# Kernel optimization log

Measured on AMD Instinct MI355X. Metric: run time of the kernel, lower is better.

Reference implementation:

```python
import jax, jax.numpy as jnp
import numpy as np

N = 100000   # nodes
E = 3200000  # edges per graph
D = 16       # embedding_size, num_heads = 1
ATTN_SLOPE = 0.2   # DGL GATv2Conv negative_slope default
ACT_SLOPE = 0.01   # torch.nn.functional.leaky_relu default (activation arg)


def gatv2_layer(h, src, dst, W_src, b_src, W_dst, b_dst, attn):
    """DGL GATv2Conv with num_heads=1, activation=leaky_relu.
    h: [N, D]; src/dst: [E] int; W_*: [D, D]; b_*: [D]; attn: [D].
    """
    feat_src = h @ W_src + b_src          # [N, D]
    feat_dst = h @ W_dst + b_dst          # [N, D]
    el = feat_src[src]                    # [E, D] gather to edges
    e = jax.nn.leaky_relu(el + feat_dst[dst], ATTN_SLOPE)  # [E, D]
    score = e @ attn                      # [E] attention logits
    # segment softmax over incoming edges of each destination node
    smax = jax.ops.segment_max(score, dst, num_segments=N)
    smax = jnp.where(jnp.isfinite(smax), smax, 0.0)  # empty segments -> 0
    ex = jnp.exp(score - smax[dst])       # [E]
    denom = jax.ops.segment_sum(ex, dst, num_segments=N)  # [N]
    alpha = ex / denom[dst]               # [E]
    rst = jax.ops.segment_sum(alpha[:, None] * el, dst, num_segments=N)  # [N, D]
    return jax.nn.leaky_relu(rst, ACT_SLOPE)


def setup_inputs() -> dict:
    key = jax.random.key(0)
    ks = jax.random.split(key, 16)
    s = 1.0 / np.sqrt(D)
    return {
        "embedding": jax.random.normal(ks[0], (N, D), jnp.float32),
        "src1": jax.random.randint(ks[1], (E,), 0, N, jnp.int32),
        "dst1": jax.random.randint(ks[2], (E,), 0, N, jnp.int32),
        "src2": jax.random.randint(ks[3], (E,), 0, N, jnp.int32),
        "dst2": jax.random.randint(ks[4], (E,), 0, N, jnp.int32),
        "W_src1": jax.random.normal(ks[5], (D, D), jnp.float32) * s,
        "b_src1": jnp.zeros((D,), jnp.float32),
        "W_dst1": jax.random.normal(ks[6], (D, D), jnp.float32) * s,
        "b_dst1": jnp.zeros((D,), jnp.float32),
        "attn1": jax.random.normal(ks[7], (D,), jnp.float32) * s,
        "W_src2": jax.random.normal(ks[8], (D, D), jnp.float32) * s,
        "b_src2": jnp.zeros((D,), jnp.float32),
        "W_dst2": jax.random.normal(ks[9], (D, D), jnp.float32) * s,
        "b_dst2": jnp.zeros((D,), jnp.float32),
        "attn2": jax.random.normal(ks[10], (D,), jnp.float32) * s,
    }


def reference(embedding, src1, dst1, src2, dst2,
              W_src1, b_src1, W_dst1, b_dst1, attn1,
              W_src2, b_src2, W_dst2, b_dst2, attn2):
    user2item = gatv2_layer(embedding, src1, dst1, W_src1, b_src1, W_dst1, b_dst1, attn1)
    item_influence = gatv2_layer(user2item, src2, dst2, W_src2, b_src2, W_dst2, b_dst2, attn2)
    return item_influence  # [N, D]
```

## Files before the change

kernel.cpp:

```cpp
#include <hip/hip_runtime.h>
#include <hip/hip_fp16.h>

#define D 16
#define R 64
#define RBITS 6
#define RMASK 63
#define STRIDE 2560
#define CAP 2560
#define KPT (CAP / 256)
#define EPB 8192
#define SBT 1024
#define NBMAX 2048
#define ATTN_SLOPE 0.2f
#define ACT_SLOPE 0.01f

__device__ __forceinline__ float leaky_a(float v) {
    return v > 0.f ? v : ATTN_SLOPE * v;
}

__device__ __forceinline__ float2 h2f(unsigned u) {
    __half2 h = *(__half2*)&u;
    return __half22float2(h);
}

__device__ __forceinline__ int block_scan_pair(int pair, int tid, int* swsum) {
    int lane = tid & 63, w = tid >> 6;
    int x = pair;
#pragma unroll
    for (int ofs = 1; ofs < 64; ofs <<= 1) {
        int y = __shfl_up(x, ofs, 64);
        if (lane >= ofs) x += y;
    }
    if (lane == 63) swsum[w] = x;
    __syncthreads();
    if (w == 0) {
        int v = (lane < 16) ? swsum[lane] : 0;
        int s = v;
#pragma unroll
        for (int ofs = 1; ofs < 16; ofs <<= 1) {
            int y = __shfl_up(s, ofs, 64);
            if (lane >= ofs) s += y;
        }
        if (lane < 16) swsum[lane] = s - v;
    }
    __syncthreads();
    return x - pair + swsum[w];
}

__global__ void node_transform_kernel(const float* __restrict__ h,
                                      const float* __restrict__ Wsrc,
                                      const float* __restrict__ bsrc,
                                      const float* __restrict__ Wdst,
                                      const float* __restrict__ bdst,
                                      __half* __restrict__ feat_src_h,
                                      float* __restrict__ feat_dst,
                                      int* __restrict__ gcur,
                                      int N, int NB) {
    __shared__ float sWs[D * D], sWd[D * D], sbs[D], sbd[D];
    int t = threadIdx.x;
    if (t < D * D) {
        sWs[t] = Wsrc[t];
        sWd[t] = Wdst[t];
    }
    if (t < D) {
        sbs[t] = bsrc[t];
        sbd[t] = bdst[t];
    }
    int n = blockIdx.x * blockDim.x + t;
    if (n < NB) gcur[n] = n * STRIDE;
    __syncthreads();
    if (n >= N) return;
    float hv[D];
    const float4* h4 = (const float4*)(h + (size_t)n * D);
#pragma unroll
    for (int k = 0; k < 4; k++) {
        float4 v = h4[k];
        hv[4 * k] = v.x; hv[4 * k + 1] = v.y; hv[4 * k + 2] = v.z; hv[4 * k + 3] = v.w;
    }
    float os[D], od[D];
#pragma unroll
    for (int d = 0; d < D; d++) {
        float ss = sbs[d];
        float sd = sbd[d];
#pragma unroll
        for (int k = 0; k < D; k++) {
            ss += hv[k] * sWs[k * D + d];
            sd += hv[k] * sWd[k * D + d];
        }
        os[d] = ss; od[d] = sd;
    }
    unsigned us[8];
#pragma unroll
    for (int k = 0; k < 8; k++) {
        __half2 hh = __floats2half2_rn(os[2 * k], os[2 * k + 1]);
        us[k] = *(unsigned*)&hh;
    }
    uint4* fo = (uint4*)(feat_src_h + (size_t)n * D);
    fo[0] = make_uint4(us[0], us[1], us[2], us[3]);
    fo[1] = make_uint4(us[4], us[5], us[6], us[7]);
    float4* fd4 = (float4*)(feat_dst + (size_t)n * D);
#pragma unroll
    for (int k = 0; k < 4; k++)
        fd4[k] = make_float4(od[4 * k], od[4 * k + 1], od[4 * k + 2], od[4 * k + 3]);
}

__global__ void binscatter_kernel(const int* __restrict__ src, const int* __restrict__ dst,
                                  int* __restrict__ gcur, unsigned* __restrict__ binned,
                                  int E, int NB) {
    __shared__ unsigned sorted[EPB];
    __shared__ unsigned short sposb[EPB];
    __shared__ int shist[NBMAX];
    __shared__ int soffs[NBMAX];
    __shared__ int sgbase[NBMAX];
    __shared__ int swsum[16];
    int tid = threadIdx.x;
    int base = blockIdx.x * EPB;
    int count = E - base;
    if (count > EPB) count = EPB;

    for (int i = tid; i < NB; i += SBT) shist[i] = 0;
    __syncthreads();
    if (base + EPB <= E) {
        const int4* d4 = (const int4*)(dst + base);
#pragma unroll
        for (int k = 0; k < EPB / SBT / 4; k++) {
            int4 v = d4[k * SBT + tid];
            atomicAdd(&shist[v.x >> RBITS], 1);
            atomicAdd(&shist[v.y >> RBITS], 1);
            atomicAdd(&shist[v.z >> RBITS], 1);
            atomicAdd(&shist[v.w >> RBITS], 1);
        }
    } else {
#pragma unroll
        for (int k = 0; k < EPB / SBT; k++) {
            int e = base + k * SBT + tid;
            if (e < E) atomicAdd(&shist[dst[e] >> RBITS], 1);
        }
    }
    __syncthreads();
    int i0 = 2 * tid, i1 = 2 * tid + 1;
    int a0 = (i0 < NB) ? shist[i0] : 0;
    int a1 = (i1 < NB) ? shist[i1] : 0;
    int excl = block_scan_pair(a0 + a1, tid, swsum);
    if (i0 < NB) {
        shist[i0] = excl;
        soffs[i0] = excl;
        if (a0 > 0) sgbase[i0] = atomicAdd(&gcur[i0], a0);
    }
    if (i1 < NB) {
        shist[i1] = excl + a0;
        soffs[i1] = excl + a0;
        if (a1 > 0) sgbase[i1] = atomicAdd(&gcur[i1], a1);
    }
    __syncthreads();
    if (base + EPB <= E) {
        const int4* s4 = (const int4*)(src + base);
        const int4* d4 = (const int4*)(dst + base);
#pragma unroll
        for (int k = 0; k < EPB / SBT / 4; k++) {
            int4 sv = s4[k * SBT + tid];
            int4 dv = d4[k * SBT + tid];
            int ss[4] = {sv.x, sv.y, sv.z, sv.w};
            int dd[4] = {dv.x, dv.y, dv.z, dv.w};
#pragma unroll
            for (int m = 0; m < 4; m++) {
                int b = dd[m] >> RBITS;
                int r = atomicAdd(&soffs[b], 1);
                sorted[r] = ((unsigned)ss[m] << RBITS) | (unsigned)(dd[m] & RMASK);
                sposb[r] = (unsigned short)b;
            }
        }
    } else {
#pragma unroll
        for (int k = 0; k < EPB / SBT; k++) {
            int e = base + k * SBT + tid;
            if (e < E) {
                int dv = dst[e];
                int b = dv >> RBITS;
                int r = atomicAdd(&soffs[b], 1);
                sorted[r] = ((unsigned)src[e] << RBITS) | (unsigned)(dv & RMASK);
                sposb[r] = (unsigned short)b;
            }
        }
    }
    __syncthreads();
#pragma unroll
    for (int k = 0; k < EPB / SBT; k++) {
        int p = k * SBT + tid;
        if (p < count) {
            int bb = sposb[p];
            int pos = sgbase[bb] + (p - shist[bb]);
            if (pos < (bb + 1) * STRIDE) binned[pos] = sorted[p];
        }
    }
}

__global__ void __launch_bounds__(256)
accumulate_kernel(const unsigned* __restrict__ binned,
                  const int* __restrict__ gcur,
                  const __half* __restrict__ feat_src_h,
                  const float* __restrict__ feat_dst,
                  const float* __restrict__ attn,
                  float* __restrict__ out, int N) {
    __shared__ float sfd[R * D];
    __shared__ int ebuf[CAP];
    __shared__ float exbuf[CAP];
    __shared__ int cstart[R + 1];
    __shared__ int cur[R];
    int b = blockIdx.x;
    int tid = threadIdx.x;
    int node0 = b * R;
    int nn = N - node0;
    if (nn > R) nn = R;
    for (int i = tid; i < nn * D; i += 256) sfd[i] = feat_dst[node0 * D + i];
    if (tid <= R) cstart[tid] = 0;

    float av[D];
#pragma unroll
    for (int k = 0; k < D; k++) av[k] = attn[k];

    int base = b * STRIDE;
    int cnt = gcur[b] - base;
    if (cnt > CAP) cnt = CAP;

    unsigned pls[KPT];
#pragma unroll
    for (int k = 0; k < KPT; k++) {
        int j = k * 256 + tid;
        pls[k] = (j < cnt) ? binned[base + j] : 0xFFFFFFFFu;
    }
    __syncthreads();

    const uint4* fsh4 = (const uint4*)feat_src_h;
    const uint2* fsq = (const uint2*)feat_src_h;
    const float4* sfd4 = (const float4*)sfd;

#pragma unroll
    for (int k = 0; k < KPT; k++)
        if (pls[k] != 0xFFFFFFFFu) atomicAdd(&cstart[pls[k] & RMASK], 1);

    float exs[KPT];
#pragma unroll
    for (int k = 0; k < KPT; k += 2) {
        unsigned q0 = pls[k], q1 = pls[k + 1];
        uint4 ua0, ub0, ua1, ub1;
        if (q0 != 0xFFFFFFFFu) {
            int s = q0 >> RBITS;
            ua0 = fsh4[2 * s]; ub0 = fsh4[2 * s + 1];
        }
        if (q1 != 0xFFFFFFFFu) {
            int s = q1 >> RBITS;
            ua1 = fsh4[2 * s]; ub1 = fsh4[2 * s + 1];
        }
        if (q0 != 0xFFFFFFFFu) {
            int loc = q0 & RMASK;
            float4 f0 = sfd4[loc * 4 + 0], f1 = sfd4[loc * 4 + 1];
            float4 f2 = sfd4[loc * 4 + 2], f3 = sfd4[loc * 4 + 3];
            float2 c0 = h2f(ua0.x), c1 = h2f(ua0.y), c2 = h2f(ua0.z), c3 = h2f(ua0.w);
            float2 c4 = h2f(ub0.x), c5 = h2f(ub0.y), c6 = h2f(ub0.z), c7 = h2f(ub0.w);
            float p = leaky_a(c0.x + f0.x) * av[0]  + leaky_a(c0.y + f0.y) * av[1]
                    + leaky_a(c1.x + f0.z) * av[2]  + leaky_a(c1.y + f0.w) * av[3]
                    + leaky_a(c2.x + f1.x) * av[4]  + leaky_a(c2.y + f1.y) * av[5]
                    + leaky_a(c3.x + f1.z) * av[6]  + leaky_a(c3.y + f1.w) * av[7]
                    + leaky_a(c4.x + f2.x) * av[8]  + leaky_a(c4.y + f2.y) * av[9]
                    + leaky_a(c5.x + f2.z) * av[10] + leaky_a(c5.y + f2.w) * av[11]
                    + leaky_a(c6.x + f3.x) * av[12] + leaky_a(c6.y + f3.y) * av[13]
                    + leaky_a(c7.x + f3.z) * av[14] + leaky_a(c7.y + f3.w) * av[15];
            exs[k] = __expf(p);
        }
        if (q1 != 0xFFFFFFFFu) {
            int loc = q1 & RMASK;
            float4 f0 = sfd4[loc * 4 + 0], f1 = sfd4[loc * 4 + 1];
            float4 f2 = sfd4[loc * 4 + 2], f3 = sfd4[loc * 4 + 3];
            float2 c0 = h2f(ua1.x), c1 = h2f(ua1.y), c2 = h2f(ua1.z), c3 = h2f(ua1.w);
            float2 c4 = h2f(ub1.x), c5 = h2f(ub1.y), c6 = h2f(ub1.z), c7 = h2f(ub1.w);
            float p = leaky_a(c0.x + f0.x) * av[0]  + leaky_a(c0.y + f0.y) * av[1]
                    + leaky_a(c1.x + f0.z) * av[2]  + leaky_a(c1.y + f0.w) * av[3]
                    + leaky_a(c2.x + f1.x) * av[4]  + leaky_a(c2.y + f1.y) * av[5]
                    + leaky_a(c3.x + f1.z) * av[6]  + leaky_a(c3.y + f1.w) * av[7]
                    + leaky_a(c4.x + f2.x) * av[8]  + leaky_a(c4.y + f2.y) * av[9]
                    + leaky_a(c5.x + f2.z) * av[10] + leaky_a(c5.y + f2.w) * av[11]
                    + leaky_a(c6.x + f3.x) * av[12] + leaky_a(c6.y + f3.y) * av[13]
                    + leaky_a(c7.x + f3.z) * av[14] + leaky_a(c7.y + f3.w) * av[15];
            exs[k + 1] = __expf(p);
        }
    }
    __syncthreads();
    if (tid < R) {
        int v = cstart[tid];
        int x = v;
#pragma unroll
        for (int ofs = 1; ofs < 64; ofs <<= 1) {
            int y = __shfl_up(x, ofs, 64);
            if (tid >= ofs) x += y;
        }
        cstart[tid] = x - v;
        cur[tid] = x - v;
        if (tid == R - 1) cstart[R] = x;
    }
    __syncthreads();
#pragma unroll
    for (int k = 0; k < KPT; k++) {
        unsigned pl = pls[k];
        if (pl != 0xFFFFFFFFu) {
            int r = atomicAdd(&cur[pl & RMASK], 1);
            ebuf[r] = (int)pl;
            exbuf[r] = exs[k];
        }
    }
    __syncthreads();

    int lane = tid & 63;
    int w = tid >> 6;
    int q = lane & 3;
    int s2 = (lane >> 2) & 3;
    int n2 = lane >> 4;

    float4 acc[4];
    float den[4];
#pragma unroll
    for (int i = 0; i < 4; i++) {
        acc[i] = make_float4(0.f, 0.f, 0.f, 0.f);
        den[i] = 0.f;
    }
#pragma unroll
    for (int i = 0; i < 4; i++) {
        int loc = w * 16 + i * 4 + n2;
        int kb = cstart[loc], ke = cstart[loc + 1];
        int k = kb + s2;
        for (; k + 12 < ke; k += 16) {
            int pl0 = ebuf[k];
            int pl1 = ebuf[k + 4];
            int pl2 = ebuf[k + 8];
            int pl3 = ebuf[k + 12];
            float ex0 = exbuf[k];
            float ex1 = exbuf[k + 4];
            float ex2 = exbuf[k + 8];
            float ex3 = exbuf[k + 12];
            uint2 u0 = fsq[(((unsigned)pl0) >> RBITS) * 4 + q];
            uint2 u1 = fsq[(((unsigned)pl1) >> RBITS) * 4 + q];
            uint2 u2 = fsq[(((unsigned)pl2) >> RBITS) * 4 + q];
            uint2 u3 = fsq[(((unsigned)pl3) >> RBITS) * 4 + q];
            float2 a01 = h2f(u0.x), a23 = h2f(u0.y);
            float2 b01 = h2f(u1.x), b23 = h2f(u1.y);
            float2 c01 = h2f(u2.x), c23 = h2f(u2.y);
            float2 d01 = h2f(u3.x), d23 = h2f(u3.y);
            acc[i].x += ex0 * a01.x + ex1 * b01.x + ex2 * c01.x + ex3 * d01.x;
            acc[i].y += ex0 * a01.y + ex1 * b01.y + ex2 * c01.y + ex3 * d01.y;
            acc[i].z += ex0 * a23.x + ex1 * b23.x + ex2 * c23.x + ex3 * d23.x;
            acc[i].w += ex0 * a23.y + ex1 * b23.y + ex2 * c23.y + ex3 * d23.y;
            den[i] += (ex0 + ex1) + (ex2 + ex3);
        }
        for (; k < ke; k += 4) {
            int pl = ebuf[k];
            float ex = exbuf[k];
            uint2 u = fsq[(((unsigned)pl) >> RBITS) * 4 + q];
            float2 a01 = h2f(u.x), a23 = h2f(u.y);
            acc[i].x += ex * a01.x;
            acc[i].y += ex * a01.y;
            acc[i].z += ex * a23.x;
            acc[i].w += ex * a23.y;
            den[i] += ex;
        }
    }
#pragma unroll
    for (int i = 0; i < 4; i++) {
        float4 a = acc[i];
        float dn = den[i];
#pragma unroll
        for (int m = 4; m <= 8; m <<= 1) {
            a.x += __shfl_xor(a.x, m, 16);
            a.y += __shfl_xor(a.y, m, 16);
            a.z += __shfl_xor(a.z, m, 16);
            a.w += __shfl_xor(a.w, m, 16);
            dn += __shfl_xor(dn, m, 16);
        }
        int loc = w * 16 + i * 4 + n2;
        if (s2 == 0 && loc < nn) {
            float inv = dn > 0.f ? 1.f / dn : 0.f;
            float4 v;
            v.x = a.x * inv; v.x = v.x > 0.f ? v.x : ACT_SLOPE * v.x;
            v.y = a.y * inv; v.y = v.y > 0.f ? v.y : ACT_SLOPE * v.y;
            v.z = a.z * inv; v.z = v.z > 0.f ? v.z : ACT_SLOPE * v.z;
            v.w = a.w * inv; v.w = v.w > 0.f ? v.w : ACT_SLOPE * v.w;
            ((float4*)out)[(size_t)(node0 + loc) * 4 + q] = v;
        }
    }
}

static void run_layer(const float* h, const int* src, const int* dst,
                      const float* Wsrc, const float* bsrc,
                      const float* Wdst, const float* bdst, const float* attn,
                      __half* feat_src_h, float* feat_dst,
                      int* gcur, unsigned* binned,
                      float* out, int N, int E, hipStream_t stream) {
    const int NB = (N + R - 1) / R;
    const int EB = (E + EPB - 1) / EPB;

    node_transform_kernel<<<(N + 255) / 256, 256, 0, stream>>>(
        h, Wsrc, bsrc, Wdst, bdst, feat_src_h, feat_dst, gcur, N, NB);

    binscatter_kernel<<<EB, SBT, 0, stream>>>(src, dst, gcur, binned, E, NB);

    accumulate_kernel<<<NB, 256, 0, stream>>>(
        binned, gcur, feat_src_h, feat_dst, attn, out, N);
}

extern "C" void kernel_launch(void* const* d_in, const int* in_sizes, int n_in,
                              void* d_out, int out_size, void* d_ws, size_t ws_size,
                              hipStream_t stream) {
    const float* emb = (const float*)d_in[0];
    const int* src1 = (const int*)d_in[1];
    const int* dst1 = (const int*)d_in[2];
    const int* src2 = (const int*)d_in[3];
    const int* dst2 = (const int*)d_in[4];
    const float* Wsrc1 = (const float*)d_in[5];
    const float* bsrc1 = (const float*)d_in[6];
    const float* Wdst1 = (const float*)d_in[7];
    const float* bdst1 = (const float*)d_in[8];
    const float* attn1 = (const float*)d_in[9];
    const float* Wsrc2 = (const float*)d_in[10];
    const float* bsrc2 = (const float*)d_in[11];
    const float* Wdst2 = (const float*)d_in[12];
    const float* bdst2 = (const float*)d_in[13];
    const float* attn2 = (const float*)d_in[14];

    const int N = in_sizes[0] / D;
    const int E1 = in_sizes[1];
    const int E2 = in_sizes[3];

    float* ws = (float*)d_ws;
    float* feat_dst = ws;
    float* h2 = feat_dst + (size_t)N * D;
    __half* feat_src_h = (__half*)(h2 + (size_t)N * D);
    int* gcur = (int*)(feat_src_h + (size_t)N * D);
    unsigned* binned = (unsigned*)(gcur + NBMAX);
    (void)ws_size; (void)n_in; (void)out_size;

    run_layer(emb, src1, dst1, Wsrc1, bsrc1, Wdst1, bdst1, attn1,
              feat_src_h, feat_dst, gcur, binned, h2, N, E1, stream);

    run_layer(h2, src2, dst2, Wsrc2, bsrc2, Wdst2, bdst2, attn2,
              feat_src_h, feat_dst, gcur, binned, (float*)d_out, N, E2, stream);
}
```

Measured before the change: 275.4 us.

## Fuse both layers' binning with transform and fold layer-2 transform into accumulate

Merges the first-layer node transform and the edge binning of both graphs into one launch, since the second graph's binning does not depend on layer-1 output. The layer-1 accumulate kernel now also applies the layer-2 linear transforms to its output nodes in shared memory, which removes the separate transform pass and the write and re-read of the intermediate embedding. Bin cursors become zero-based counters reset with a memset, and the scatter uses a precomputed per-bin delta. Binning both graphs at once needs a second binned buffer, so a fallback sequential path is kept for when the workspace is too small.

```diff
diff --git a/kernel.cpp b/kernel.cpp
--- a/kernel.cpp
+++ b/kernel.cpp
@@ -9,21 +9,56 @@
 #define CAP 2560
 #define KPT (CAP / 256)
 #define EPB 8192
-#define SBT 1024
-#define NBMAX 2048
+#define K1T 1024
+#define NB2 1664
 #define ATTN_SLOPE 0.2f
 #define ACT_SLOPE 0.01f
 
 __device__ __forceinline__ float leaky_a(float v) {
     return v > 0.f ? v : ATTN_SLOPE * v;
 }
-
 __device__ __forceinline__ float2 h2f(unsigned u) {
     __half2 h = *(__half2*)&u;
     return __half22float2(h);
 }
 
-__device__ __forceinline__ int block_scan_pair(int pair, int tid, int* swsum) {
+
+__device__ void binscatter_tile(int tile, const int* __restrict__ src,
+                                const int* __restrict__ dst,
+                                int* __restrict__ gcur, unsigned* __restrict__ binned,
+                                int E, int NB, char* sb) {
+    unsigned* sorted = (unsigned*)sb;
+    unsigned short* sposb = (unsigned short*)(sb + 32768);
+    int* soffs = (int*)(sb + 49152);
+    int* delta = (int*)(sb + 49152 + 4 * NB2);
+    int* swsum = (int*)(sb + 49152 + 8 * NB2);
+    int tid = threadIdx.x;
+    int base = tile * EPB;
+    int count = E - base;
+    if (count > EPB) count = EPB;
+    bool full = (count == EPB);
+
+    for (int i = tid; i < NB; i += K1T) soffs[i] = 0;
+    __syncthreads();
+    int dd[8];
+    if (full) {
+        const int4* d4 = (const int4*)(dst + base);
+        int4 a = d4[tid], b = d4[K1T + tid];
+        dd[0] = a.x; dd[1] = a.y; dd[2] = a.z; dd[3] = a.w;
+        dd[4] = b.x; dd[5] = b.y; dd[6] = b.z; dd[7] = b.w;
+#pragma unroll
+        for (int m = 0; m < 8; m++) atomicAdd(&soffs[dd[m] >> RBITS], 1);
+    } else {
+        for (int k = 0; k < 8; k++) {
+            int e = base + k * K1T + tid;
+            if (e < E) atomicAdd(&soffs[dst[e] >> RBITS], 1);
+        }
+    }
+    __syncthreads();
+    int i0 = 2 * tid, i1 = 2 * tid + 1;
+    int a0 = (i0 < NB) ? soffs[i0] : 0;
+    int a1 = (i1 < NB) ? soffs[i1] : 0;
+    int pair = a0 + a1;
     int lane = tid & 63, w = tid >> 6;
     int x = pair;
 #pragma unroll
@@ -44,136 +79,37 @@
         if (lane < 16) swsum[lane] = s - v;
     }
     __syncthreads();
-    return x - pair + swsum[w];
-}
-
-__global__ void node_transform_kernel(const float* __restrict__ h,
-                                      const float* __restrict__ Wsrc,
-                                      const float* __restrict__ bsrc,
-                                      const float* __restrict__ Wdst,
-                                      const float* __restrict__ bdst,
-                                      __half* __restrict__ feat_src_h,
-                                      float* __restrict__ feat_dst,
-                                      int* __restrict__ gcur,
-                                      int N, int NB) {
-    __shared__ float sWs[D * D], sWd[D * D], sbs[D], sbd[D];
-    int t = threadIdx.x;
-    if (t < D * D) {
-        sWs[t] = Wsrc[t];
-        sWd[t] = Wdst[t];
-    }
-    if (t < D) {
-        sbs[t] = bsrc[t];
-        sbd[t] = bdst[t];
-    }
-    int n = blockIdx.x * blockDim.x + t;
-    if (n < NB) gcur[n] = n * STRIDE;
-    __syncthreads();
-    if (n >= N) return;
-    float hv[D];
-    const float4* h4 = (const float4*)(h + (size_t)n * D);
-#pragma unroll
-    for (int k = 0; k < 4; k++) {
-        float4 v = h4[k];
-        hv[4 * k] = v.x; hv[4 * k + 1] = v.y; hv[4 * k + 2] = v.z; hv[4 * k + 3] = v.w;
-    }
-    float os[D], od[D];
-#pragma unroll
-    for (int d = 0; d < D; d++) {
-        float ss = sbs[d];
-        float sd = sbd[d];
-#pragma unroll
-        for (int k = 0; k < D; k++) {
-            ss += hv[k] * sWs[k * D + d];
-            sd += hv[k] * sWd[k * D + d];
-        }
-        os[d] = ss; od[d] = sd;
-    }
-    unsigned us[8];
-#pragma unroll
-    for (int k = 0; k < 8; k++) {
-        __half2 hh = __floats2half2_rn(os[2 * k], os[2 * k + 1]);
-        us[k] = *(unsigned*)&hh;
-    }
-    uint4* fo = (uint4*)(feat_src_h + (size_t)n * D);
-    fo[0] = make_uint4(us[0], us[1], us[2], us[3]);
-    fo[1] = make_uint4(us[4], us[5], us[6], us[7]);
-    float4* fd4 = (float4*)(feat_dst + (size_t)n * D);
-#pragma unroll
-    for (int k = 0; k < 4; k++)
-        fd4[k] = make_float4(od[4 * k], od[4 * k + 1], od[4 * k + 2], od[4 * k + 3]);
-}
-
-__global__ void binscatter_kernel(const int* __restrict__ src, const int* __restrict__ dst,
-                                  int* __restrict__ gcur, unsigned* __restrict__ binned,
-                                  int E, int NB) {
-    __shared__ unsigned sorted[EPB];
-    __shared__ unsigned short sposb[EPB];
-    __shared__ int shist[NBMAX];
-    __shared__ int soffs[NBMAX];
-    __shared__ int sgbase[NBMAX];
-    __shared__ int swsum[16];
-    int tid = threadIdx.x;
-    int base = blockIdx.x * EPB;
-    int count = E - base;
-    if (count > EPB) count = EPB;
-
-    for (int i = tid; i < NB; i += SBT) shist[i] = 0;
-    __syncthreads();
-    if (base + EPB <= E) {
-        const int4* d4 = (const int4*)(dst + base);
-#pragma unroll
-        for (int k = 0; k < EPB / SBT / 4; k++) {
-            int4 v = d4[k * SBT + tid];
-            atomicAdd(&shist[v.x >> RBITS], 1);
-            atomicAdd(&shist[v.y >> RBITS], 1);
-            atomicAdd(&shist[v.z >> RBITS], 1);
-            atomicAdd(&shist[v.w >> RBITS], 1);
+    int excl = x - pair + swsum[w];
+    __syncthreads();
+    if (i0 < NB) {
+        soffs[i0] = excl;
+        if (a0 > 0) {
+            int res = atomicAdd(&gcur[i0], a0);
+            delta[i0] = i0 * STRIDE + res - excl;
+        }
+    }
+    if (i1 < NB) {
+        soffs[i1] = excl + a0;
+        if (a1 > 0) {
+            int res = atomicAdd(&gcur[i1], a1);
+            delta[i1] = i1 * STRIDE + res - (excl + a0);
+        }
+    }
+    __syncthreads();
+    if (full) {
+        const int4* s4 = (const int4*)(src + base);
+        int4 sa = s4[tid], sb4 = s4[K1T + tid];
+        int ss[8] = {sa.x, sa.y, sa.z, sa.w, sb4.x, sb4.y, sb4.z, sb4.w};
+#pragma unroll
+        for (int m = 0; m < 8; m++) {
+            int b = dd[m] >> RBITS;
+            int r = atomicAdd(&soffs[b], 1);
+            sorted[r] = ((unsigned)ss[m] << RBITS) | (unsigned)(dd[m] & RMASK);
+            sposb[r] = (unsigned short)b;
         }
     } else {
-#pragma unroll
-        for (int k = 0; k < EPB / SBT; k++) {
-            int e = base + k * SBT + tid;
-            if (e < E) atomicAdd(&shist[dst[e] >> RBITS], 1);
-        }
-    }
-    __syncthreads();
-    int i0 = 2 * tid, i1 = 2 * tid + 1;
-    int a0 = (i0 < NB) ? shist[i0] : 0;
-    int a1 = (i1 < NB) ? shist[i1] : 0;
-    int excl = block_scan_pair(a0 + a1, tid, swsum);
-    if (i0 < NB) {
-        shist[i0] = excl;
-        soffs[i0] = excl;
-        if (a0 > 0) sgbase[i0] = atomicAdd(&gcur[i0], a0);
-    }
-    if (i1 < NB) {
-        shist[i1] = excl + a0;
-        soffs[i1] = excl + a0;
-        if (a1 > 0) sgbase[i1] = atomicAdd(&gcur[i1], a1);
-    }
-    __syncthreads();
-    if (base + EPB <= E) {
-        const int4* s4 = (const int4*)(src + base);
-        const int4* d4 = (const int4*)(dst + base);
-#pragma unroll
-        for (int k = 0; k < EPB / SBT / 4; k++) {
-            int4 sv = s4[k * SBT + tid];
-            int4 dv = d4[k * SBT + tid];
-            int ss[4] = {sv.x, sv.y, sv.z, sv.w};
-            int dd[4] = {dv.x, dv.y, dv.z, dv.w};
-#pragma unroll
-            for (int m = 0; m < 4; m++) {
-                int b = dd[m] >> RBITS;
-                int r = atomicAdd(&soffs[b], 1);
-                sorted[r] = ((unsigned)ss[m] << RBITS) | (unsigned)(dd[m] & RMASK);
-                sposb[r] = (unsigned short)b;
-            }
-        }
-    } else {
-#pragma unroll
-        for (int k = 0; k < EPB / SBT; k++) {
-            int e = base + k * SBT + tid;
+        for (int k = 0; k < 8; k++) {
+            int e = base + k * K1T + tid;
             if (e < E) {
                 int dv = dst[e];
                 int b = dv >> RBITS;
@@ -185,23 +121,94 @@
     }
     __syncthreads();
 #pragma unroll
-    for (int k = 0; k < EPB / SBT; k++) {
-        int p = k * SBT + tid;
+    for (int m = 0; m < 8; m++) {
+        int p = m * K1T + tid;
         if (p < count) {
-            int bb = sposb[p];
-            int pos = sgbase[bb] + (p - shist[bb]);
-            if (pos < (bb + 1) * STRIDE) binned[pos] = sorted[p];
-        }
-    }
-}
-
+            int b = sposb[p];
+            int pos = p + delta[b];
+            if (pos < (b + 1) * STRIDE) binned[pos] = sorted[p];
+        }
+    }
+}
+
+__device__ void transform_tile(int tile, const float* __restrict__ h,
+                               const float* __restrict__ Ws, const float* __restrict__ bs,
+                               const float* __restrict__ Wd, const float* __restrict__ bd,
+                               __half* __restrict__ fsh, float* __restrict__ fdst,
+                               int N, char* sb) {
+    float* sWs = (float*)sb;
+    float* sWd = sWs + 256;
+    float* sbs = sWd + 256;
+    float* sbd = sbs + 16;
+    int t = threadIdx.x;
+    if (t < 256) { sWs[t] = Ws[t]; sWd[t] = Wd[t]; }
+    if (t < 16) { sbs[t] = bs[t]; sbd[t] = bd[t]; }
+    __syncthreads();
+    int n = tile * K1T + t;
+    if (n >= N) return;
+    float hv[D];
+    const float4* h4 = (const float4*)(h + (size_t)n * D);
+#pragma unroll
+    for (int k = 0; k < 4; k++) {
+        float4 v = h4[k];
+        hv[4 * k] = v.x; hv[4 * k + 1] = v.y; hv[4 * k + 2] = v.z; hv[4 * k + 3] = v.w;
+    }
+    float os[D], od[D];
+#pragma unroll
+    for (int d = 0; d < D; d++) {
+        float ss = sbs[d];
+        float sd = sbd[d];
+#pragma unroll
+        for (int k = 0; k < D; k++) {
+            ss += hv[k] * sWs[k * D + d];
+            sd += hv[k] * sWd[k * D + d];
+        }
+        os[d] = ss; od[d] = sd;
+    }
+    unsigned us[8];
+#pragma unroll
+    for (int k = 0; k < 8; k++) {
+        __half2 hh = __floats2half2_rn(os[2 * k], os[2 * k + 1]);
+        us[k] = *(unsigned*)&hh;
+    }
+    uint4* fo = (uint4*)(fsh + (size_t)n * D);
+    fo[0] = make_uint4(us[0], us[1], us[2], us[3]);
+    fo[1] = make_uint4(us[4], us[5], us[6], us[7]);
+    float4* fd4 = (float4*)(fdst + (size_t)n * D);
+#pragma unroll
+    for (int k = 0; k < 4; k++)
+        fd4[k] = make_float4(od[4 * k], od[4 * k + 1], od[4 * k + 2], od[4 * k + 3]);
+}
+
+__global__ void __launch_bounds__(K1T)
+k1_kernel(const float* h, const float* Ws, const float* bs,
+          const float* Wd, const float* bd,
+          __half* fsh, float* fdst,
+          const int* srcA, const int* dstA, int* gA, unsigned* binnedA, int EA,
+          const int* srcB, const int* dstB, int* gB, unsigned* binnedB, int EB,
+          int N, int NB, int B1, int B2, int TT) {
+    __shared__ __align__(16) char sb[49152 + 8 * NB2 + 64];
+    int bid = blockIdx.x;
+    if (bid < B1) {
+        binscatter_tile(bid, srcA, dstA, gA, binnedA, EA, NB, sb);
+    } else if (bid < B1 + B2) {
+        binscatter_tile(bid - B1, srcB, dstB, gB, binnedB, EB, NB, sb);
+    } else {
+        int t = bid - B1 - B2;
+        if (t < TT) transform_tile(t, h, Ws, bs, Wd, bd, fsh, fdst, N, sb);
+    }
+}
+
+
+template <bool DO_TAIL>
 __global__ void __launch_bounds__(256)
-accumulate_kernel(const unsigned* __restrict__ binned,
-                  const int* __restrict__ gcur,
-                  const __half* __restrict__ feat_src_h,
-                  const float* __restrict__ feat_dst,
-                  const float* __restrict__ attn,
-                  float* __restrict__ out, int N) {
+acc_kernel(const unsigned* __restrict__ binned, const int* __restrict__ gcur,
+           const __half* __restrict__ fsh, const float* __restrict__ fdst,
+           const float* __restrict__ attn, float* __restrict__ out,
+           __half* __restrict__ fs2h, float* __restrict__ fd2,
+           const float* __restrict__ Ws2, const float* __restrict__ bs2,
+           const float* __restrict__ Wd2, const float* __restrict__ bd2,
+           int N) {
     __shared__ float sfd[R * D];
     __shared__ int ebuf[CAP];
     __shared__ float exbuf[CAP];
@@ -212,16 +219,16 @@
     int node0 = b * R;
     int nn = N - node0;
     if (nn > R) nn = R;
-    for (int i = tid; i < nn * D; i += 256) sfd[i] = feat_dst[node0 * D + i];
+    for (int i = tid; i < nn * D; i += 256) sfd[i] = fdst[node0 * D + i];
     if (tid <= R) cstart[tid] = 0;
 
     float av[D];
 #pragma unroll
     for (int k = 0; k < D; k++) av[k] = attn[k];
 
+    int cnt = gcur[b];
+    if (cnt > CAP) cnt = CAP;
     int base = b * STRIDE;
-    int cnt = gcur[b] - base;
-    if (cnt > CAP) cnt = CAP;
 
     unsigned pls[KPT];
 #pragma unroll
@@ -231,8 +238,8 @@
     }
     __syncthreads();
 
-    const uint4* fsh4 = (const uint4*)feat_src_h;
-    const uint2* fsq = (const uint2*)feat_src_h;
+    const uint4* fsh4 = (const uint4*)fsh;
+    const uint2* fsq = (const uint2*)fsh;
     const float4* sfd4 = (const float4*)sfd;
 
 #pragma unroll
@@ -383,28 +390,45 @@
             v.y = a.y * inv; v.y = v.y > 0.f ? v.y : ACT_SLOPE * v.y;
             v.z = a.z * inv; v.z = v.z > 0.f ? v.z : ACT_SLOPE * v.z;
             v.w = a.w * inv; v.w = v.w > 0.f ? v.w : ACT_SLOPE * v.w;
-            ((float4*)out)[(size_t)(node0 + loc) * 4 + q] = v;
-        }
-    }
-}
-
-static void run_layer(const float* h, const int* src, const int* dst,
-                      const float* Wsrc, const float* bsrc,
-                      const float* Wdst, const float* bdst, const float* attn,
-                      __half* feat_src_h, float* feat_dst,
-                      int* gcur, unsigned* binned,
-                      float* out, int N, int E, hipStream_t stream) {
-    const int NB = (N + R - 1) / R;
-    const int EB = (E + EPB - 1) / EPB;
-
-    node_transform_kernel<<<(N + 255) / 256, 256, 0, stream>>>(
-        h, Wsrc, bsrc, Wdst, bdst, feat_src_h, feat_dst, gcur, N, NB);
-
-    binscatter_kernel<<<EB, SBT, 0, stream>>>(src, dst, gcur, binned, E, NB);
-
-    accumulate_kernel<<<NB, 256, 0, stream>>>(
-        binned, gcur, feat_src_h, feat_dst, attn, out, N);
-}
+            if (DO_TAIL) {
+                *(float4*)&sfd[loc * D + q * 4] = v;
+            } else {
+                ((float4*)out)[(size_t)(node0 + loc) * 4 + q] = v;
+            }
+        }
+    }
+    if (DO_TAIL) {
+        __syncthreads();
+        float* wb = (float*)ebuf;
+        if (tid < 256) { wb[tid] = Ws2[tid]; wb[256 + tid] = Wd2[tid]; }
+        if (tid < 16) { wb[512 + tid] = bs2[tid]; wb[528 + tid] = bd2[tid]; }
+        __syncthreads();
+        int loc = tid >> 2, qq = tid & 3;
+        if (loc < nn) {
+            float hvv[16];
+#pragma unroll
+            for (int k = 0; k < 16; k++) hvv[k] = sfd[loc * D + k];
+            float s0 = wb[512 + 4 * qq], s1 = wb[513 + 4 * qq];
+            float s2v = wb[514 + 4 * qq], s3 = wb[515 + 4 * qq];
+            float d0 = wb[528 + 4 * qq], d1 = wb[529 + 4 * qq];
+            float d2v = wb[530 + 4 * qq], d3 = wb[531 + 4 * qq];
+#pragma unroll
+            for (int k = 0; k < 16; k++) {
+                float hk = hvv[k];
+                const float* wr = &wb[k * 16 + 4 * qq];
+                const float* wr2 = &wb[256 + k * 16 + 4 * qq];
+                s0 += hk * wr[0]; s1 += hk * wr[1]; s2v += hk * wr[2]; s3 += hk * wr[3];
+                d0 += hk * wr2[0]; d1 += hk * wr2[1]; d2v += hk * wr2[2]; d3 += hk * wr2[3];
+            }
+            __half2 p0 = __floats2half2_rn(s0, s1), p1 = __floats2half2_rn(s2v, s3);
+            *(uint2*)(fs2h + (size_t)(node0 + loc) * D + 4 * qq) =
+                make_uint2(*(unsigned*)&p0, *(unsigned*)&p1);
+            *(float4*)(fd2 + (size_t)(node0 + loc) * D + 4 * qq) =
+                make_float4(d0, d1, d2v, d3);
+        }
+    }
+}
+
 
 extern "C" void kernel_launch(void* const* d_in, const int* in_sizes, int n_in,
                               void* d_out, int out_size, void* d_ws, size_t ws_size,
@@ -428,18 +452,56 @@
     const int N = in_sizes[0] / D;
     const int E1 = in_sizes[1];
     const int E2 = in_sizes[3];
+    const int NB = (N + R - 1) / R;
+    const size_t ndf = (size_t)N * D;
 
     float* ws = (float*)d_ws;
-    float* feat_dst = ws;
-    float* h2 = feat_dst + (size_t)N * D;
-    __half* feat_src_h = (__half*)(h2 + (size_t)N * D);
-    int* gcur = (int*)(feat_src_h + (size_t)N * D);
-    unsigned* binned = (unsigned*)(gcur + NBMAX);
-    (void)ws_size; (void)n_in; (void)out_size;
-
-    run_layer(emb, src1, dst1, Wsrc1, bsrc1, Wdst1, bdst1, attn1,
-              feat_src_h, feat_dst, gcur, binned, h2, N, E1, stream);
-
-    run_layer(h2, src2, dst2, Wsrc2, bsrc2, Wdst2, bdst2, attn2,
-              feat_src_h, feat_dst, gcur, binned, (float*)d_out, N, E2, stream);
-}
+    float* fd1 = ws;
+    float* fd2 = fd1 + ndf;
+    __half* fs1h = (__half*)(fd2 + ndf);
+    __half* fs2h = fs1h + ndf;
+    int* gA = (int*)(fs2h + ndf);
+    int* gB = gA + NB2;
+    unsigned* binned1 = (unsigned*)(gB + NB2);
+    unsigned* binned2big = binned1 + (size_t)NB * STRIDE;
+    size_t bigNeed = (size_t)((char*)(binned2big + (size_t)NB * STRIDE) - (char*)d_ws);
+    bool big = ws_size >= bigNeed;
+    (void)n_in; (void)out_size;
+
+    const int B1 = (E1 + EPB - 1) / EPB;
+    const int B2 = (E2 + EPB - 1) / EPB;
+    const int TT = (N + K1T - 1) / K1T;
+
+    (void)hipMemsetAsync(gA, 0, 2 * NB2 * sizeof(int), stream);
+
+    if (big) {
+        k1_kernel<<<B1 + B2 + TT, K1T, 0, stream>>>(
+            emb, Wsrc1, bsrc1, Wdst1, bdst1, fs1h, fd1,
+            src1, dst1, gA, binned1, E1,
+            src2, dst2, gB, binned2big, E2,
+            N, NB, B1, B2, TT);
+        acc_kernel<true><<<NB, 256, 0, stream>>>(
+            binned1, gA, fs1h, fd1, attn1, nullptr,
+            fs2h, fd2, Wsrc2, bsrc2, Wdst2, bdst2, N);
+        acc_kernel<false><<<NB, 256, 0, stream>>>(
+            binned2big, gB, fs2h, fd2, attn2, (float*)d_out,
+            nullptr, nullptr, nullptr, nullptr, nullptr, nullptr, N);
+    } else {
+        k1_kernel<<<B1 + TT, K1T, 0, stream>>>(
+            emb, Wsrc1, bsrc1, Wdst1, bdst1, fs1h, fd1,
+            src1, dst1, gA, binned1, E1,
+            src2, dst2, gB, binned1, 0,
+            N, NB, B1, 0, TT);
+        acc_kernel<true><<<NB, 256, 0, stream>>>(
+            binned1, gA, fs1h, fd1, attn1, nullptr,
+            fs2h, fd2, Wsrc2, bsrc2, Wdst2, bdst2, N);
+        k1_kernel<<<B2, K1T, 0, stream>>>(
+            emb, Wsrc1, bsrc1, Wdst1, bdst1, fs1h, fd1,
+            src2, dst2, gB, binned1, E2,
+            src2, dst2, gB, binned1, 0,
+            N, NB, B2, 0, 0);
+        acc_kernel<false><<<NB, 256, 0, stream>>>(
+            binned1, gB, fs2h, fd2, attn2, (float*)d_out,
+            nullptr, nullptr, nullptr, nullptr, nullptr, nullptr, N);
+    }
+}
```

Result: faster. 241.7 us (median of 2 runs) (-12.2%).
